# Kernel optimization log

Hardware: AMD Instinct MI355X
Metric: run time of the kernel (lower is better)

## Reference

```python
import jax, jax.numpy as jnp
import numpy as np

N_NODES, N_EDGES, N_GRAPHS = 20000, 320000, 8
NFD, HID, OUT, HEADS = 128, 64, 768, 4


def gat_conv(x, src, dst, ea, W, att_src, att_dst, We, att_edge, bias, heads, concat):
    """PyG GATConv with edge_dim, add_self_loops=True (fill_value='mean'), eval mode."""
    N = x.shape[0]
    H = heads
    C = W.shape[1] // H
    loop = jnp.arange(N, dtype=src.dtype)
    s = jnp.concatenate([src, loop])
    d = jnp.concatenate([dst, loop])
    ea_full = jnp.concatenate([ea, jnp.broadcast_to(ea.mean(axis=0), (N, ea.shape[1]))], axis=0)
    h = (x @ W).reshape(N, H, C)                      # [N,H,C]
    a_s = (h * att_src).sum(-1)                        # [N,H]
    a_d = (h * att_dst).sum(-1)                        # [N,H]
    eh = (ea_full @ We).reshape(-1, H, C)              # [Etot,H,C]
    a_e = (eh * att_edge).sum(-1)                      # [Etot,H]
    logit = jax.nn.leaky_relu(a_s[s] + a_d[d] + a_e, negative_slope=0.2)
    m = jax.ops.segment_max(logit, d, num_segments=N)  # segment softmax over dst
    w = jnp.exp(logit - m[d])
    z = jax.ops.segment_sum(w, d, num_segments=N)
    alpha = w / (z[d] + 1e-16)                         # [Etot,H]
    out = jax.ops.segment_sum(h[s] * alpha[:, :, None], d, num_segments=N)
    out = out.reshape(N, H * C) if concat else out.mean(axis=1)
    return out + bias


def setup_inputs() -> dict:
    key = jax.random.key(0)
    ks = jax.random.split(key, 32)
    p = lambda k, shp: (jax.random.normal(k, shp) * 0.1).astype(jnp.float32)
    inp = {
        'x': jax.random.normal(ks[0], (N_NODES, 5), dtype=jnp.float32),
        'edge_index': jax.random.randint(ks[1], (2, N_EDGES), 0, N_NODES, dtype=jnp.int32),
        'edge_attr': jax.random.uniform(ks[2], (N_EDGES, 4), dtype=jnp.float32),
        'batch': jnp.sort(jax.random.randint(ks[3], (N_NODES,), 0, N_GRAPHS, dtype=jnp.int32)),
        # node_encoder
        'enc_w1': p(ks[4], (5, NFD // 2)), 'enc_b1': jnp.zeros((NFD // 2,), jnp.float32),
        'enc_w2': p(ks[5], (NFD // 2, NFD)), 'enc_b2': jnp.zeros((NFD,), jnp.float32),
        # gat1: in NFD -> HEADS*HID (concat)
        'g1_w': p(ks[6], (NFD, HEADS * HID)), 'g1_asrc': p(ks[7], (HEADS, HID)),
        'g1_adst': p(ks[8], (HEADS, HID)), 'g1_we': p(ks[9], (4, HEADS * HID)),
        'g1_aedge': p(ks[10], (HEADS, HID)), 'g1_b': jnp.zeros((HEADS * HID,), jnp.float32),
        # gat2: in HEADS*HID -> HEADS*HID (concat)
        'g2_w': p(ks[11], (HEADS * HID, HEADS * HID)), 'g2_asrc': p(ks[12], (HEADS, HID)),
        'g2_adst': p(ks[13], (HEADS, HID)), 'g2_we': p(ks[14], (4, HEADS * HID)),
        'g2_aedge': p(ks[15], (HEADS, HID)), 'g2_b': jnp.zeros((HEADS * HID,), jnp.float32),
        # gat3: in HEADS*HID -> HID, heads=1, concat=False
        'g3_w': p(ks[16], (HEADS * HID, HID)), 'g3_asrc': p(ks[17], (1, HID)),
        'g3_adst': p(ks[18], (1, HID)), 'g3_we': p(ks[19], (4, HID)),
        'g3_aedge': p(ks[20], (1, HID)), 'g3_b': jnp.zeros((HID,), jnp.float32),
        # projection HID -> 2*HID -> OUT
        'proj_w1': p(ks[21], (HID, 2 * HID)), 'proj_b1': jnp.zeros((2 * HID,), jnp.float32),
        'proj_w2': p(ks[22], (2 * HID, OUT)), 'proj_b2': jnp.zeros((OUT,), jnp.float32),
        # 5 vulnerability heads stacked: OUT -> 5
        'vuln_w': p(ks[23], (OUT, 5)), 'vuln_b': jnp.zeros((5,), jnp.float32),
    }
    return inp


def reference(x, edge_index, edge_attr, batch,
              enc_w1, enc_b1, enc_w2, enc_b2,
              g1_w, g1_asrc, g1_adst, g1_we, g1_aedge, g1_b,
              g2_w, g2_asrc, g2_adst, g2_we, g2_aedge, g2_b,
              g3_w, g3_asrc, g3_adst, g3_we, g3_aedge, g3_b,
              proj_w1, proj_b1, proj_w2, proj_b2, vuln_w, vuln_b):
    src, dst = edge_index[0], edge_index[1]
    # node_encoder (eval mode, dropout = identity)
    h = jax.nn.relu(x @ enc_w1 + enc_b1)
    h = jax.nn.relu(h @ enc_w2 + enc_b2)                         # [N, NFD]
    # EdgeAwareGAT
    h = jax.nn.elu(gat_conv(h, src, dst, edge_attr, g1_w, g1_asrc, g1_adst, g1_we, g1_aedge, g1_b, HEADS, True))
    h = jax.nn.elu(gat_conv(h, src, dst, edge_attr, g2_w, g2_asrc, g2_adst, g2_we, g2_aedge, g2_b, HEADS, True))
    h = gat_conv(h, src, dst, edge_attr, g3_w, g3_asrc, g3_adst, g3_we, g3_aedge, g3_b, 1, False)  # [N, HID]
    # global_mean_pool
    sums = jax.ops.segment_sum(h, batch, num_segments=N_GRAPHS)
    cnts = jax.ops.segment_sum(jnp.ones((h.shape[0], 1), h.dtype), batch, num_segments=N_GRAPHS)
    g = sums / jnp.maximum(cnts, 1.0)                            # [B, HID]
    # projection
    p1 = jax.nn.relu(g @ proj_w1 + proj_b1)
    static_features = p1 @ proj_w2 + proj_b2                     # [B, OUT]
    scores = jax.nn.sigmoid(static_features @ vuln_w + vuln_b)   # [B, 5]
    return static_features, scores
```

## Files before the change

kernel.cpp:

```cpp
#include <hip/hip_runtime.h>
#include <hip/hip_bf16.h>
#include <hip/hip_fp16.h>
#include <math.h>

#define N_NODES 20000
#define M_PAD 20096
#define N_EDGES 320000
#define N_GRAPHS 8

typedef _Float16 half8 __attribute__((ext_vector_type(8)));
typedef float floatx4 __attribute__((ext_vector_type(4)));

__device__ __forceinline__ float leaky02(float x) { return x > 0.f ? x : 0.2f * x; }
__device__ __forceinline__ float sel4(int hl, float a, float b, float c, float d) {
    return hl < 2 ? (hl == 0 ? a : b) : (hl == 2 ? c : d);
}

__global__ void encoder_kernel(const float* __restrict__ x,
                               const float* __restrict__ w1, const float* __restrict__ b1,
                               const float* __restrict__ w2, const float* __restrict__ b2,
                               __half* __restrict__ out) {
    const int n0 = blockIdx.x * 8;
    const int tid = threadIdx.x;
    __shared__ float s_x[8][5];
    __shared__ float s_h1[8][64];
    if (tid < 40) s_x[tid / 5][tid % 5] = x[(size_t)(n0 + tid / 5) * 5 + (tid % 5)];
    __syncthreads();
    if (tid < 64) {
        #pragma unroll
        for (int n = 0; n < 8; ++n) {
            float a = b1[tid];
            #pragma unroll
            for (int k = 0; k < 5; ++k) a += s_x[n][k] * w1[k * 64 + tid];
            s_h1[n][tid] = fmaxf(a, 0.f);
        }
    }
    __syncthreads();
    float acc[8];
    #pragma unroll
    for (int n = 0; n < 8; ++n) acc[n] = b2[tid];
    for (int k = 0; k < 64; ++k) {
        float wv = w2[k * 128 + tid];
        #pragma unroll
        for (int n = 0; n < 8; ++n) acc[n] += s_h1[n][k] * wv;
    }
    #pragma unroll
    for (int n = 0; n < 8; ++n)
        out[(size_t)(n0 + n) * 128 + tid] = __float2half(fmaxf(acc[n], 0.f));
}

__global__ void ea_sum_kernel(const float* __restrict__ ea, float* __restrict__ ea_sum) {
    const int tid = threadIdx.x;
    float a0 = 0, a1 = 0, a2 = 0, a3 = 0;
    for (int i = blockIdx.x * blockDim.x + tid; i < N_EDGES; i += gridDim.x * blockDim.x) {
        float4 v = ((const float4*)ea)[i];
        a0 += v.x; a1 += v.y; a2 += v.z; a3 += v.w;
    }
    #pragma unroll
    for (int off = 32; off; off >>= 1) {
        a0 += __shfl_down(a0, off, 64);
        a1 += __shfl_down(a1, off, 64);
        a2 += __shfl_down(a2, off, 64);
        a3 += __shfl_down(a3, off, 64);
    }
    __shared__ float s[4][4];
    const int wave = tid >> 6, lane = tid & 63;
    if (lane == 0) { s[wave][0] = a0; s[wave][1] = a1; s[wave][2] = a2; s[wave][3] = a3; }
    __syncthreads();
    if (tid < 4) {
        float t = s[0][tid] + s[1][tid] + s[2][tid] + s[3][tid];
        atomicAdd(&ea_sum[tid], t);
    }
}

__global__ void count_kernel(const int* __restrict__ dst, int* __restrict__ cnt) {
    int i = blockIdx.x * 256 + threadIdx.x;
    if (i < N_EDGES) atomicAdd(&cnt[dst[i]], 1);
}

__global__ void scan_kernel(const int* __restrict__ cnt, int* __restrict__ row_ptr) {
    __shared__ int s_sum[1024];
    const int tid = threadIdx.x;
    int local[20];
    int run = 0;
    const int base = tid * 20;
    #pragma unroll
    for (int i = 0; i < 20; ++i) {
        int idx = base + i;
        int v = (idx < N_NODES) ? cnt[idx] : 0;
        run += v;
        local[i] = run;
    }
    s_sum[tid] = run;
    __syncthreads();
    for (int off = 1; off < 1024; off <<= 1) {
        int v = (tid >= off) ? s_sum[tid - off] : 0;
        __syncthreads();
        s_sum[tid] += v;
        __syncthreads();
    }
    const int prev = (tid > 0) ? s_sum[tid - 1] : 0;
    #pragma unroll
    for (int i = 0; i < 20; ++i) {
        int idx = base + i;
        if (idx < N_NODES) row_ptr[idx + 1] = prev + local[i];
    }
    if (tid == 0) row_ptr[0] = 0;
}

__global__ void scatter_kernel(const int* __restrict__ dst, const int* __restrict__ row_ptr,
                               int* __restrict__ cur, int* __restrict__ eid) {
    int i = blockIdx.x * 256 + threadIdx.x;
    if (i < N_EDGES) {
        int d = dst[i];
        int p = atomicAdd(&cur[d], 1);
        eid[row_ptr[d] + p] = i;
    }
}

__global__ void csr_gather_kernel(const int* __restrict__ srcs, const float* __restrict__ ea,
                                  const int* __restrict__ eids,
                                  int* __restrict__ csr_src, float* __restrict__ csr_ea) {
    int e = blockIdx.x * 256 + threadIdx.x;
    if (e < N_EDGES) {
        int ei = eids[e];
        csr_src[e] = srcs[ei];
        ((float4*)csr_ea)[e] = ((const float4*)ea)[ei];
    }
}

__global__ void wconv_kernel(const float* __restrict__ W, __half* __restrict__ Wt,
                             int K, int N) {
    int i = blockIdx.x * 256 + threadIdx.x;
    if (i < K * N) {
        int k = i / N, n = i % N;
        Wt[(size_t)n * K + k] = __float2half(W[i]);
    }
}

template<int H>
__global__ void vtab_kernel(const float* __restrict__ We, const float* __restrict__ att_edge,
                            const float* __restrict__ ea_sum,
                            float* __restrict__ vtab, float* __restrict__ lpae) {
    const int tid = threadIdx.x;
    __shared__ float s_v[4][4];
    if (tid < 4 * H) {
        const int k = tid / H, h = tid % H;
        float v = 0.f;
        for (int c = 0; c < 64; ++c) v += We[k * (H * 64) + h * 64 + c] * att_edge[h * 64 + c];
        vtab[k * 4 + h] = v;
        s_v[k][h] = v;
    }
    __syncthreads();
    if (tid < H) {
        const float inv = 1.0f / (float)N_EDGES;
        float l = 0.f;
        #pragma unroll
        for (int k = 0; k < 4; ++k) l += ea_sum[k] * inv * s_v[k][tid];
        lpae[tid] = l;
    }
}

template<int N, int H>
__global__ __launch_bounds__(256) void mgemm_kernel(
    const __half* __restrict__ X, const __half* __restrict__ Wt,
    const float* __restrict__ asrc, const float* __restrict__ adst,
    __half* __restrict__ Y, float* __restrict__ a_s, float* __restrict__ a_d, int K) {
    constexpr int STR = 72;
    __shared__ _Float16 sX[64 * STR];
    __shared__ _Float16 sW[64 * STR];
    const int tid = threadIdx.x;
    const int lane = tid & 63, w = tid >> 6;
    const int l16 = lane & 15, kg = lane >> 4;
    const int n0 = blockIdx.x * 64;
    const int c0 = blockIdx.y * 64;
    const int by = blockIdx.y;

    floatx4 acc[4];
    #pragma unroll
    for (int ct = 0; ct < 4; ++ct) acc[ct] = (floatx4){0.f, 0.f, 0.f, 0.f};

    const int srow = tid >> 2, sseg = tid & 3;
    for (int k0 = 0; k0 < K; k0 += 32) {
        float4 xv = *(const float4*)(X + (size_t)(n0 + srow) * K + k0 + sseg * 8);
        float4 wv = *(const float4*)(Wt + (size_t)(c0 + srow) * K + k0 + sseg * 8);
        __syncthreads();
        *(float4*)&sX[srow * STR + sseg * 8] = xv;
        *(float4*)&sW[srow * STR + sseg * 8] = wv;
        __syncthreads();
        half8 a = *(const half8*)&sX[(w * 16 + l16) * STR + kg * 8];
        #pragma unroll
        for (int ct = 0; ct < 4; ++ct) {
            half8 b = *(const half8*)&sW[(ct * 16 + l16) * STR + kg * 8];
            acc[ct] = __builtin_amdgcn_mfma_f32_16x16x32_f16(a, b, acc[ct], 0, 0, 0);
        }
    }

    const int rowb = n0 + w * 16 + kg * 4;
    float ar[4], ad4[4];
    #pragma unroll
    for (int ct = 0; ct < 4; ++ct) {
        ar[ct] = asrc[c0 + ct * 16 + l16];
        ad4[ct] = adst[c0 + ct * 16 + l16];
    }
    #pragma unroll
    for (int ct = 0; ct < 4; ++ct) {
        const int col = c0 + ct * 16 + l16;
        #pragma unroll
        for (int r = 0; r < 4; ++r)
            Y[(size_t)(rowb + r) * N + col] = __float2half(acc[ct][r]);
    }
    #pragma unroll
    for (int r = 0; r < 4; ++r) {
        float p = acc[0][r] * ar[0] + acc[1][r] * ar[1] + acc[2][r] * ar[2] + acc[3][r] * ar[3];
        float q = acc[0][r] * ad4[0] + acc[1][r] * ad4[1] + acc[2][r] * ad4[2] + acc[3][r] * ad4[3];
        #pragma unroll
        for (int off = 1; off < 16; off <<= 1) {
            p += __shfl_xor(p, off, 64);
            q += __shfl_xor(q, off, 64);
        }
        if (l16 == 0) {
            const int node = rowb + r;
            a_s[(size_t)node * H + by] = p;
            a_d[(size_t)node * H + by] = q;
        }
    }
}

template<int H, int HC, bool ELU>
__global__ __launch_bounds__(256) void agg3_kernel(
    const __half* __restrict__ hh,
    const float* __restrict__ a_s, const float* __restrict__ a_d,
    const float* __restrict__ vtab, const float* __restrict__ lpae,
    const int* __restrict__ csr_src, const float* __restrict__ csr_ea,
    const int* __restrict__ row_ptr, const float* __restrict__ bias,
    __half* __restrict__ out) {
    constexpr int CPT = HC / 64;
    const int wave = threadIdx.x >> 6;
    const int lane = threadIdx.x & 63;
    const int d = blockIdx.x * 4 + wave;

    const int base = row_ptr[d], end = row_ptr[d + 1];
    const int colbase = lane * CPT;
    const int hl = (H == 1) ? 0 : (colbase >> 6);

    float vt[4][H];
    #pragma unroll
    for (int k = 0; k < 4; ++k)
        #pragma unroll
        for (int h = 0; h < H; ++h) vt[k][h] = vtab[k * 4 + h];

    float add_[H];
    if (H == 4) {
        float4 t = *(const float4*)&a_d[(size_t)d * 4];
        add_[0] = t.x; add_[1] = t.y; add_[2] = t.z; add_[3] = t.w;
    } else {
        add_[0] = a_d[d];
    }
    float asd_h;
    if (H == 4) asd_h = a_s[(size_t)d * 4 + hl];
    else asd_h = a_s[d];

    float mh = leaky02(asd_h + add_[hl] + lpae[hl]);
    float zacc = 1.f;
    float acc[CPT];
    {
        const __half2* hp = (const __half2*)(hh + (size_t)d * HC + colbase);
        if (CPT == 4) {
            float2 f0 = __half22float2(hp[0]);
            float2 f1 = __half22float2(hp[1]);
            acc[0] = f0.x; acc[1] = f0.y; acc[2] = f1.x; acc[3] = f1.y;
        } else {
            acc[0] = __half2float(hh[(size_t)d * HC + colbase]);
        }
    }

#define EDGE_STEP(tt) { \
        int s_ = __shfl(my_s, (tt), 64); \
        float lt; \
        if (H == 4) { \
            float t0 = __shfl(l0, (tt), 64), t1 = __shfl(l1, (tt), 64); \
            float t2 = __shfl(l2, (tt), 64), t3 = __shfl(l3, (tt), 64); \
            lt = sel4(hl, t0, t1, t2, t3); \
        } else { \
            lt = __shfl(l0, (tt), 64); \
        } \
        float w_ = __expf(lt - mh); \
        const __half2* hp_ = (const __half2*)(hh + (size_t)s_ * HC + colbase); \
        if (CPT == 4) { \
            float2 f0_ = __half22float2(hp_[0]); \
            float2 f1_ = __half22float2(hp_[1]); \
            acc[0] += w_ * f0_.x; acc[1] += w_ * f0_.y; \
            acc[2] += w_ * f1_.x; acc[3] += w_ * f1_.y; \
        } else { \
            acc[0] += w_ * __half2float(hh[(size_t)s_ * HC + colbase]); \
        } \
        zacc += w_; }

    for (int c0 = base; c0 < end; c0 += 64) {
        const int nc = min(64, end - c0);
        int my_s = 0;
        float l0 = -1e30f, l1 = -1e30f, l2 = -1e30f, l3 = -1e30f;
        if (lane < nc) {
            my_s = csr_src[c0 + lane];
            float4 eav = ((const float4*)csr_ea)[c0 + lane];
            if (H == 4) {
                float4 as4 = *(const float4*)&a_s[(size_t)my_s * 4];
                l0 = leaky02(as4.x + add_[0] + eav.x * vt[0][0] + eav.y * vt[1][0] + eav.z * vt[2][0] + eav.w * vt[3][0]);
                l1 = leaky02(as4.y + add_[1] + eav.x * vt[0][1] + eav.y * vt[1][1] + eav.z * vt[2][1] + eav.w * vt[3][1]);
                l2 = leaky02(as4.z + add_[2] + eav.x * vt[0][2] + eav.y * vt[1][2] + eav.z * vt[2][2] + eav.w * vt[3][2]);
                l3 = leaky02(as4.w + add_[3] + eav.x * vt[0][3] + eav.y * vt[1][3] + eav.z * vt[2][3] + eav.w * vt[3][3]);
            } else {
                l0 = leaky02(a_s[my_s] + add_[0] + eav.x * vt[0][0] + eav.y * vt[1][0] + eav.z * vt[2][0] + eav.w * vt[3][0]);
            }
        }
        float cm0 = l0, cm1 = l1, cm2 = l2, cm3 = l3;
        #pragma unroll
        for (int off = 1; off < 64; off <<= 1) {
            cm0 = fmaxf(cm0, __shfl_xor(cm0, off, 64));
            if (H == 4) {
                cm1 = fmaxf(cm1, __shfl_xor(cm1, off, 64));
                cm2 = fmaxf(cm2, __shfl_xor(cm2, off, 64));
                cm3 = fmaxf(cm3, __shfl_xor(cm3, off, 64));
            }
        }
        float cmh = (H == 4) ? sel4(hl, cm0, cm1, cm2, cm3) : cm0;
        float newm = fmaxf(mh, cmh);
        float sc = __expf(mh - newm);
        zacc *= sc;
        #pragma unroll
        for (int c = 0; c < CPT; ++c) acc[c] *= sc;
        mh = newm;

        int t = 0;
        for (; t + 4 <= nc; t += 4) {
            EDGE_STEP(t)
            EDGE_STEP(t + 1)
            EDGE_STEP(t + 2)
            EDGE_STEP(t + 3)
        }
        for (; t < nc; ++t) {
            EDGE_STEP(t)
        }
    }
#undef EDGE_STEP

    const float invz = 1.f / (zacc + 1e-16f);
    #pragma unroll
    for (int c = 0; c < CPT; ++c) {
        float v = acc[c] * invz + bias[colbase + c];
        if (ELU) v = (v > 0.f) ? v : (__expf(v) - 1.f);
        acc[c] = v;
    }
    if (CPT == 4) {
        __half2* op = (__half2*)(out + (size_t)d * HC + colbase);
        op[0] = __floats2half2_rn(acc[0], acc[1]);
        op[1] = __floats2half2_rn(acc[2], acc[3]);
    } else {
        out[(size_t)d * HC + colbase] = __float2half(acc[0]);
    }
}

__global__ void pool_kernel(const __half* __restrict__ h3, const int* __restrict__ batch,
                            float* __restrict__ psum, float* __restrict__ pcnt) {
    __shared__ float s_acc[8][64];
    __shared__ float s_cnt[8];
    const int tid = threadIdx.x;
    for (int i = tid; i < 512; i += 256) s_acc[i >> 6][i & 63] = 0.f;
    if (tid < 8) s_cnt[tid] = 0.f;
    __syncthreads();
    const int col = tid & 63, nl = tid >> 6;
    const int n0 = blockIdx.x * 64;
    for (int nn = nl; nn < 64; nn += 4) {
        int n = n0 + nn;
        if (n < N_NODES) {
            int b = batch[n];
            atomicAdd(&s_acc[b][col], __half2float(h3[(size_t)n * 64 + col]));
            if (col == 0) atomicAdd(&s_cnt[b], 1.0f);
        }
    }
    __syncthreads();
    for (int i = tid; i < 512; i += 256) {
        float v = s_acc[i >> 6][i & 63];
        if (v != 0.f) atomicAdd(&psum[i], v);
    }
    if (tid < 8 && s_cnt[tid] > 0.f) atomicAdd(&pcnt[tid], s_cnt[tid]);
}

__global__ void head_sf_kernel(const float* __restrict__ psum, const float* __restrict__ pcnt,
                               const float* __restrict__ w1, const float* __restrict__ b1,
                               const float* __restrict__ w2, const float* __restrict__ b2,
                               float* __restrict__ out) {
    const int b = blockIdx.y;
    const int c0 = blockIdx.x * 128;
    const int tid = threadIdx.x;
    __shared__ float s_g[64];
    __shared__ float s_p1[128];
    if (tid < 64) {
        float c = pcnt[b];
        c = (c < 1.f) ? 1.f : c;
        s_g[tid] = psum[b * 64 + tid] / c;
    }
    __syncthreads();
    {
        float a = b1[tid];
        #pragma unroll 8
        for (int k = 0; k < 64; ++k) a += s_g[k] * w1[k * 128 + tid];
        s_p1[tid] = fmaxf(a, 0.f);
    }
    __syncthreads();
    const int col = c0 + tid;
    float a = b2[col];
    #pragma unroll 8
    for (int k = 0; k < 128; ++k) a += s_p1[k] * w2[k * 768 + col];
    out[b * 768 + col] = a;
}

__global__ void scores_kernel(const float* __restrict__ sf,
                              const float* __restrict__ vw, const float* __restrict__ vb,
                              float* __restrict__ out) {
    const int b = blockIdx.x;
    const int tid = threadIdx.x;
    const int wave = tid >> 6, lane = tid & 63;
    float part[5] = {0.f, 0.f, 0.f, 0.f, 0.f};
    for (int k = tid; k < 768; k += 256) {
        float s = sf[b * 768 + k];
        #pragma unroll
        for (int v = 0; v < 5; ++v) part[v] += s * vw[k * 5 + v];
    }
    #pragma unroll
    for (int v = 0; v < 5; ++v)
        #pragma unroll
        for (int off = 32; off; off >>= 1) part[v] += __shfl_down(part[v], off, 64);
    __shared__ float sred[4][5];
    if (lane == 0) {
        #pragma unroll
        for (int v = 0; v < 5; ++v) sred[wave][v] = part[v];
    }
    __syncthreads();
    if (tid < 5) {
        float a = vb[tid] + sred[0][tid] + sred[1][tid] + sred[2][tid] + sred[3][tid];
        out[6144 + b * 5 + tid] = 1.f / (1.f + __expf(-a));
    }
}

extern "C" void kernel_launch(void* const* d_in, const int* in_sizes, int n_in,
                              void* d_out, int out_size, void* d_ws, size_t ws_size,
                              hipStream_t stream) {
    const float* x       = (const float*)d_in[0];
    const int*   eidx    = (const int*)d_in[1];
    const float* ea      = (const float*)d_in[2];
    const int*   batch   = (const int*)d_in[3];
    const float* enc_w1  = (const float*)d_in[4];
    const float* enc_b1  = (const float*)d_in[5];
    const float* enc_w2  = (const float*)d_in[6];
    const float* enc_b2  = (const float*)d_in[7];
    const float* g1_w    = (const float*)d_in[8];
    const float* g1_asrc = (const float*)d_in[9];
    const float* g1_adst = (const float*)d_in[10];
    const float* g1_we   = (const float*)d_in[11];
    const float* g1_ae   = (const float*)d_in[12];
    const float* g1_b    = (const float*)d_in[13];
    const float* g2_w    = (const float*)d_in[14];
    const float* g2_asrc = (const float*)d_in[15];
    const float* g2_adst = (const float*)d_in[16];
    const float* g2_we   = (const float*)d_in[17];
    const float* g2_ae   = (const float*)d_in[18];
    const float* g2_b    = (const float*)d_in[19];
    const float* g3_w    = (const float*)d_in[20];
    const float* g3_asrc = (const float*)d_in[21];
    const float* g3_adst = (const float*)d_in[22];
    const float* g3_we   = (const float*)d_in[23];
    const float* g3_ae   = (const float*)d_in[24];
    const float* g3_b    = (const float*)d_in[25];
    const float* pw1     = (const float*)d_in[26];
    const float* pb1     = (const float*)d_in[27];
    const float* pw2     = (const float*)d_in[28];
    const float* pb2     = (const float*)d_in[29];
    const float* vw      = (const float*)d_in[30];
    const float* vb      = (const float*)d_in[31];

    const int* src = eidx;
    const int* dst = eidx + N_EDGES;

    __half* h16a = (__half*)d_ws;
    __half* h16b = h16a + (size_t)M_PAD * 256;
    __half* hh16 = h16b + (size_t)M_PAD * 256;
    __half* wt16 = hh16 + (size_t)M_PAD * 256;
    float* asb   = (float*)(wt16 + 256 * 256);
    float* adb   = asb + (size_t)M_PAD * 4;
    float* zreg  = adb + (size_t)M_PAD * 4;
    float* ea_sum = zreg;
    float* psum   = zreg + 4;
    float* pcnt   = zreg + 516;
    float* vtab  = zreg + 524;
    float* lpae  = vtab + 16;
    int* icnt    = (int*)(lpae + 4);
    int* icur    = icnt + N_NODES;
    int* irow    = icur + N_NODES;
    int* ieid    = irow + N_NODES + 4;
    int* csr_src = ieid + N_EDGES;
    float* csr_ea = (float*)(csr_src + N_EDGES);

    hipMemsetAsync(zreg, 0, 544 * sizeof(float), stream);
    hipMemsetAsync(icnt, 0, 2 * N_NODES * sizeof(int), stream);

    ea_sum_kernel<<<256, 256, 0, stream>>>(ea, ea_sum);
    encoder_kernel<<<N_NODES / 8, 128, 0, stream>>>(x, enc_w1, enc_b1, enc_w2, enc_b2, h16a);
    count_kernel<<<(N_EDGES + 255) / 256, 256, 0, stream>>>(dst, icnt);
    scan_kernel<<<1, 1024, 0, stream>>>(icnt, irow);
    scatter_kernel<<<(N_EDGES + 255) / 256, 256, 0, stream>>>(dst, irow, icur, ieid);
    csr_gather_kernel<<<(N_EDGES + 255) / 256, 256, 0, stream>>>(src, ea, ieid, csr_src, csr_ea);

    wconv_kernel<<<(128 * 256 + 255) / 256, 256, 0, stream>>>(g1_w, wt16, 128, 256);
    vtab_kernel<4><<<1, 64, 0, stream>>>(g1_we, g1_ae, ea_sum, vtab, lpae);
    mgemm_kernel<256, 4><<<dim3(M_PAD / 64, 4), 256, 0, stream>>>(h16a, wt16, g1_asrc, g1_adst, hh16, asb, adb, 128);
    agg3_kernel<4, 256, true><<<N_NODES / 4, 256, 0, stream>>>(hh16, asb, adb, vtab, lpae, csr_src, csr_ea, irow, g1_b, h16b);

    wconv_kernel<<<(256 * 256 + 255) / 256, 256, 0, stream>>>(g2_w, wt16, 256, 256);
    vtab_kernel<4><<<1, 64, 0, stream>>>(g2_we, g2_ae, ea_sum, vtab, lpae);
    mgemm_kernel<256, 4><<<dim3(M_PAD / 64, 4), 256, 0, stream>>>(h16b, wt16, g2_asrc, g2_adst, hh16, asb, adb, 256);
    agg3_kernel<4, 256, true><<<N_NODES / 4, 256, 0, stream>>>(hh16, asb, adb, vtab, lpae, csr_src, csr_ea, irow, g2_b, h16a);

    wconv_kernel<<<(256 * 64 + 255) / 256, 256, 0, stream>>>(g3_w, wt16, 256, 64);
    vtab_kernel<1><<<1, 64, 0, stream>>>(g3_we, g3_ae, ea_sum, vtab, lpae);
    mgemm_kernel<64, 1><<<dim3(M_PAD / 64, 1), 256, 0, stream>>>(h16a, wt16, g3_asrc, g3_adst, hh16, asb, adb, 256);
    agg3_kernel<1, 64, false><<<N_NODES / 4, 256, 0, stream>>>(hh16, asb, adb, vtab, lpae, csr_src, csr_ea, irow, g3_b, h16b);

    pool_kernel<<<(N_NODES + 63) / 64, 256, 0, stream>>>(h16b, batch, psum, pcnt);
    head_sf_kernel<<<dim3(6, 8), 128, 0, stream>>>(psum, pcnt, pw1, pb1, pw2, pb2, (float*)d_out);
    scores_kernel<<<8, 256, 0, stream>>>((float*)d_out, vw, vb, (float*)d_out);
}
```

Before: 337.3 us.

## Fuse preprocessing kernels, drop online softmax max, widen GEMM K step

Edge counting moves into the edge-attribute sum kernel, and the CSR scatter now writes source ids and edge attributes directly, so the separate eid gather pass goes away. The three weight conversions and the three vtab computations become one launch each. The GEMM loads 64 K-elements per shared-memory stage instead of 32, and the aggregation kernel unrolls by 8. The aggregation softmax now uses each node's self-loop logit as a fixed shift instead of a running max, which removes the per-chunk wave max reductions and rescaling. Without the max shift, exp can overflow if an edge logit is much larger than the self-loop logit.

```diff
diff --git a/kernel.cpp b/kernel.cpp
--- a/kernel.cpp
+++ b/kernel.cpp
@@ -10,6 +10,8 @@
 
 typedef _Float16 half8 __attribute__((ext_vector_type(8)));
 typedef float floatx4 __attribute__((ext_vector_type(4)));
+
+struct h4pack { __half2 a, b; };
 
 __device__ __forceinline__ float leaky02(float x) { return x > 0.f ? x : 0.2f * x; }
 __device__ __forceinline__ float sel4(int hl, float a, float b, float c, float d) {
@@ -49,12 +51,14 @@
         out[(size_t)(n0 + n) * 128 + tid] = __float2half(fmaxf(acc[n], 0.f));
 }
 
-__global__ void ea_sum_kernel(const float* __restrict__ ea, float* __restrict__ ea_sum) {
+__global__ void prep_kernel(const float* __restrict__ ea, const int* __restrict__ dst,
+                            float* __restrict__ ea_sum, int* __restrict__ cnt) {
     const int tid = threadIdx.x;
     float a0 = 0, a1 = 0, a2 = 0, a3 = 0;
     for (int i = blockIdx.x * blockDim.x + tid; i < N_EDGES; i += gridDim.x * blockDim.x) {
         float4 v = ((const float4*)ea)[i];
         a0 += v.x; a1 += v.y; a2 += v.z; a3 += v.w;
+        atomicAdd(&cnt[dst[i]], 1);
     }
     #pragma unroll
     for (int off = 32; off; off >>= 1) {
@@ -73,11 +77,6 @@
     }
 }
 
-__global__ void count_kernel(const int* __restrict__ dst, int* __restrict__ cnt) {
-    int i = blockIdx.x * 256 + threadIdx.x;
-    if (i < N_EDGES) atomicAdd(&cnt[dst[i]], 1);
-}
-
 __global__ void scan_kernel(const int* __restrict__ cnt, int* __restrict__ row_ptr) {
     __shared__ int s_sum[1024];
     const int tid = threadIdx.x;
@@ -108,56 +107,64 @@
     if (tid == 0) row_ptr[0] = 0;
 }
 
-__global__ void scatter_kernel(const int* __restrict__ dst, const int* __restrict__ row_ptr,
-                               int* __restrict__ cur, int* __restrict__ eid) {
+__global__ void scatter_kernel(const int* __restrict__ src, const int* __restrict__ dst,
+                               const float* __restrict__ ea,
+                               const int* __restrict__ row_ptr, int* __restrict__ cur,
+                               int* __restrict__ csr_src, float* __restrict__ csr_ea) {
     int i = blockIdx.x * 256 + threadIdx.x;
     if (i < N_EDGES) {
         int d = dst[i];
         int p = atomicAdd(&cur[d], 1);
-        eid[row_ptr[d] + p] = i;
-    }
-}
-
-__global__ void csr_gather_kernel(const int* __restrict__ srcs, const float* __restrict__ ea,
-                                  const int* __restrict__ eids,
-                                  int* __restrict__ csr_src, float* __restrict__ csr_ea) {
-    int e = blockIdx.x * 256 + threadIdx.x;
-    if (e < N_EDGES) {
-        int ei = eids[e];
-        csr_src[e] = srcs[ei];
-        ((float4*)csr_ea)[e] = ((const float4*)ea)[ei];
-    }
-}
-
-__global__ void wconv_kernel(const float* __restrict__ W, __half* __restrict__ Wt,
-                             int K, int N) {
+        int idx = row_ptr[d] + p;
+        csr_src[idx] = src[i];
+        ((float4*)csr_ea)[idx] = ((const float4*)ea)[i];
+    }
+}
+
+__global__ void wconv_all_kernel(const float* __restrict__ w1, const float* __restrict__ w2,
+                                 const float* __restrict__ w3,
+                                 __half* __restrict__ wt1, __half* __restrict__ wt2,
+                                 __half* __restrict__ wt3) {
     int i = blockIdx.x * 256 + threadIdx.x;
-    if (i < K * N) {
-        int k = i / N, n = i % N;
-        Wt[(size_t)n * K + k] = __float2half(W[i]);
-    }
-}
-
-template<int H>
-__global__ void vtab_kernel(const float* __restrict__ We, const float* __restrict__ att_edge,
-                            const float* __restrict__ ea_sum,
-                            float* __restrict__ vtab, float* __restrict__ lpae) {
-    const int tid = threadIdx.x;
-    __shared__ float s_v[4][4];
+    if (i < 32768) {
+        int k = i >> 8, n = i & 255;
+        wt1[(size_t)n * 128 + k] = __float2half(w1[i]);
+    } else if (i < 98304) {
+        int j = i - 32768;
+        int k = j >> 8, n = j & 255;
+        wt2[(size_t)n * 256 + k] = __float2half(w2[j]);
+    } else if (i < 114688) {
+        int j = i - 98304;
+        int k = j >> 6, n = j & 63;
+        wt3[(size_t)n * 256 + k] = __float2half(w3[j]);
+    }
+}
+
+__global__ void vtab_all_kernel(const float* __restrict__ we1, const float* __restrict__ ae1,
+                                const float* __restrict__ we2, const float* __restrict__ ae2,
+                                const float* __restrict__ we3, const float* __restrict__ ae3,
+                                const float* __restrict__ ea_sum,
+                                float* __restrict__ vtab, float* __restrict__ lpae) {
+    const int L = blockIdx.x;
+    const float* We = (L == 0) ? we1 : ((L == 1) ? we2 : we3);
+    const float* Ae = (L == 0) ? ae1 : ((L == 1) ? ae2 : ae3);
+    const int H = (L < 2) ? 4 : 1;
+    const int tid = threadIdx.x;
+    __shared__ float s_v[16];
     if (tid < 4 * H) {
         const int k = tid / H, h = tid % H;
         float v = 0.f;
-        for (int c = 0; c < 64; ++c) v += We[k * (H * 64) + h * 64 + c] * att_edge[h * 64 + c];
-        vtab[k * 4 + h] = v;
-        s_v[k][h] = v;
+        for (int c = 0; c < 64; ++c) v += We[k * (H * 64) + h * 64 + c] * Ae[h * 64 + c];
+        vtab[L * 16 + k * 4 + h] = v;
+        s_v[k * 4 + h] = v;
     }
     __syncthreads();
     if (tid < H) {
         const float inv = 1.0f / (float)N_EDGES;
         float l = 0.f;
         #pragma unroll
-        for (int k = 0; k < 4; ++k) l += ea_sum[k] * inv * s_v[k][tid];
-        lpae[tid] = l;
+        for (int k = 0; k < 4; ++k) l += ea_sum[k] * inv * s_v[k * 4 + tid];
+        lpae[L * 4 + tid] = l;
     }
 }
 
@@ -181,18 +188,25 @@
     for (int ct = 0; ct < 4; ++ct) acc[ct] = (floatx4){0.f, 0.f, 0.f, 0.f};
 
     const int srow = tid >> 2, sseg = tid & 3;
-    for (int k0 = 0; k0 < K; k0 += 32) {
-        float4 xv = *(const float4*)(X + (size_t)(n0 + srow) * K + k0 + sseg * 8);
-        float4 wv = *(const float4*)(Wt + (size_t)(c0 + srow) * K + k0 + sseg * 8);
+    for (int k0 = 0; k0 < K; k0 += 64) {
+        float4 xv0 = *(const float4*)(X + (size_t)(n0 + srow) * K + k0 + sseg * 8);
+        float4 xv1 = *(const float4*)(X + (size_t)(n0 + srow) * K + k0 + 32 + sseg * 8);
+        float4 wv0 = *(const float4*)(Wt + (size_t)(c0 + srow) * K + k0 + sseg * 8);
+        float4 wv1 = *(const float4*)(Wt + (size_t)(c0 + srow) * K + k0 + 32 + sseg * 8);
         __syncthreads();
-        *(float4*)&sX[srow * STR + sseg * 8] = xv;
-        *(float4*)&sW[srow * STR + sseg * 8] = wv;
+        *(float4*)&sX[srow * STR + sseg * 8] = xv0;
+        *(float4*)&sX[srow * STR + 32 + sseg * 8] = xv1;
+        *(float4*)&sW[srow * STR + sseg * 8] = wv0;
+        *(float4*)&sW[srow * STR + 32 + sseg * 8] = wv1;
         __syncthreads();
-        half8 a = *(const half8*)&sX[(w * 16 + l16) * STR + kg * 8];
-        #pragma unroll
-        for (int ct = 0; ct < 4; ++ct) {
-            half8 b = *(const half8*)&sW[(ct * 16 + l16) * STR + kg * 8];
-            acc[ct] = __builtin_amdgcn_mfma_f32_16x16x32_f16(a, b, acc[ct], 0, 0, 0);
+        #pragma unroll
+        for (int ks = 0; ks < 2; ++ks) {
+            half8 a = *(const half8*)&sX[(w * 16 + l16) * STR + ks * 32 + kg * 8];
+            #pragma unroll
+            for (int ct = 0; ct < 4; ++ct) {
+                half8 b = *(const half8*)&sW[(ct * 16 + l16) * STR + ks * 32 + kg * 8];
+                acc[ct] = __builtin_amdgcn_mfma_f32_16x16x32_f16(a, b, acc[ct], 0, 0, 0);
+            }
         }
     }
 
@@ -228,7 +242,7 @@
 }
 
 template<int H, int HC, bool ELU>
-__global__ __launch_bounds__(256) void agg3_kernel(
+__global__ __launch_bounds__(256) void agg4_kernel(
     const __half* __restrict__ hh,
     const float* __restrict__ a_s, const float* __restrict__ a_d,
     const float* __restrict__ vtab, const float* __restrict__ lpae,
@@ -250,46 +264,45 @@
         #pragma unroll
         for (int h = 0; h < H; ++h) vt[k][h] = vtab[k * 4 + h];
 
-    float add_[H];
+    float add_[H], lself[H];
     if (H == 4) {
         float4 t = *(const float4*)&a_d[(size_t)d * 4];
         add_[0] = t.x; add_[1] = t.y; add_[2] = t.z; add_[3] = t.w;
+        float4 s4 = *(const float4*)&a_s[(size_t)d * 4];
+        lself[0] = leaky02(s4.x + add_[0] + lpae[0]);
+        lself[1] = leaky02(s4.y + add_[1] + lpae[1]);
+        lself[2] = leaky02(s4.z + add_[2] + lpae[2]);
+        lself[3] = leaky02(s4.w + add_[3] + lpae[3]);
     } else {
         add_[0] = a_d[d];
-    }
-    float asd_h;
-    if (H == 4) asd_h = a_s[(size_t)d * 4 + hl];
-    else asd_h = a_s[d];
-
-    float mh = leaky02(asd_h + add_[hl] + lpae[hl]);
+        lself[0] = leaky02(a_s[d] + add_[0] + lpae[0]);
+    }
+
     float zacc = 1.f;
     float acc[CPT];
-    {
-        const __half2* hp = (const __half2*)(hh + (size_t)d * HC + colbase);
-        if (CPT == 4) {
-            float2 f0 = __half22float2(hp[0]);
-            float2 f1 = __half22float2(hp[1]);
-            acc[0] = f0.x; acc[1] = f0.y; acc[2] = f1.x; acc[3] = f1.y;
-        } else {
-            acc[0] = __half2float(hh[(size_t)d * HC + colbase]);
-        }
+    if (CPT == 4) {
+        h4pack hv = *(const h4pack*)(hh + (size_t)d * HC + colbase);
+        float2 f0 = __half22float2(hv.a);
+        float2 f1 = __half22float2(hv.b);
+        acc[0] = f0.x; acc[1] = f0.y; acc[2] = f1.x; acc[3] = f1.y;
+    } else {
+        acc[0] = __half2float(hh[(size_t)d * HC + colbase]);
     }
 
 #define EDGE_STEP(tt) { \
         int s_ = __shfl(my_s, (tt), 64); \
-        float lt; \
+        float w_; \
         if (H == 4) { \
-            float t0 = __shfl(l0, (tt), 64), t1 = __shfl(l1, (tt), 64); \
-            float t2 = __shfl(l2, (tt), 64), t3 = __shfl(l3, (tt), 64); \
-            lt = sel4(hl, t0, t1, t2, t3); \
+            float t0 = __shfl(w0, (tt), 64), t1 = __shfl(w1, (tt), 64); \
+            float t2 = __shfl(w2, (tt), 64), t3 = __shfl(w3, (tt), 64); \
+            w_ = sel4(hl, t0, t1, t2, t3); \
         } else { \
-            lt = __shfl(l0, (tt), 64); \
+            w_ = __shfl(w0, (tt), 64); \
         } \
-        float w_ = __expf(lt - mh); \
-        const __half2* hp_ = (const __half2*)(hh + (size_t)s_ * HC + colbase); \
         if (CPT == 4) { \
-            float2 f0_ = __half22float2(hp_[0]); \
-            float2 f1_ = __half22float2(hp_[1]); \
+            h4pack hv_ = *(const h4pack*)(hh + (size_t)s_ * HC + colbase); \
+            float2 f0_ = __half22float2(hv_.a); \
+            float2 f1_ = __half22float2(hv_.b); \
             acc[0] += w_ * f0_.x; acc[1] += w_ * f0_.y; \
             acc[2] += w_ * f1_.x; acc[3] += w_ * f1_.y; \
         } else { \
@@ -300,44 +313,35 @@
     for (int c0 = base; c0 < end; c0 += 64) {
         const int nc = min(64, end - c0);
         int my_s = 0;
-        float l0 = -1e30f, l1 = -1e30f, l2 = -1e30f, l3 = -1e30f;
+        float w0 = 0.f, w1 = 0.f, w2 = 0.f, w3 = 0.f;
         if (lane < nc) {
             my_s = csr_src[c0 + lane];
             float4 eav = ((const float4*)csr_ea)[c0 + lane];
             if (H == 4) {
                 float4 as4 = *(const float4*)&a_s[(size_t)my_s * 4];
-                l0 = leaky02(as4.x + add_[0] + eav.x * vt[0][0] + eav.y * vt[1][0] + eav.z * vt[2][0] + eav.w * vt[3][0]);
-                l1 = leaky02(as4.y + add_[1] + eav.x * vt[0][1] + eav.y * vt[1][1] + eav.z * vt[2][1] + eav.w * vt[3][1]);
-                l2 = leaky02(as4.z + add_[2] + eav.x * vt[0][2] + eav.y * vt[1][2] + eav.z * vt[2][2] + eav.w * vt[3][2]);
-                l3 = leaky02(as4.w + add_[3] + eav.x * vt[0][3] + eav.y * vt[1][3] + eav.z * vt[2][3] + eav.w * vt[3][3]);
+                float l0 = leaky02(as4.x + add_[0] + eav.x * vt[0][0] + eav.y * vt[1][0] + eav.z * vt[2][0] + eav.w * vt[3][0]);
+                float l1 = leaky02(as4.y + add_[1] + eav.x * vt[0][1] + eav.y * vt[1][1] + eav.z * vt[2][1] + eav.w * vt[3][1]);
+                float l2 = leaky02(as4.z + add_[2] + eav.x * vt[0][2] + eav.y * vt[1][2] + eav.z * vt[2][2] + eav.w * vt[3][2]);
+                float l3 = leaky02(as4.w + add_[3] + eav.x * vt[0][3] + eav.y * vt[1][3] + eav.z * vt[2][3] + eav.w * vt[3][3]);
+                w0 = __expf(l0 - lself[0]);
+                w1 = __expf(l1 - lself[1]);
+                w2 = __expf(l2 - lself[2]);
+                w3 = __expf(l3 - lself[3]);
             } else {
-                l0 = leaky02(a_s[my_s] + add_[0] + eav.x * vt[0][0] + eav.y * vt[1][0] + eav.z * vt[2][0] + eav.w * vt[3][0]);
+                float l0 = leaky02(a_s[my_s] + add_[0] + eav.x * vt[0][0] + eav.y * vt[1][0] + eav.z * vt[2][0] + eav.w * vt[3][0]);
+                w0 = __expf(l0 - lself[0]);
             }
         }
-        float cm0 = l0, cm1 = l1, cm2 = l2, cm3 = l3;
-        #pragma unroll
-        for (int off = 1; off < 64; off <<= 1) {
-            cm0 = fmaxf(cm0, __shfl_xor(cm0, off, 64));
-            if (H == 4) {
-                cm1 = fmaxf(cm1, __shfl_xor(cm1, off, 64));
-                cm2 = fmaxf(cm2, __shfl_xor(cm2, off, 64));
-                cm3 = fmaxf(cm3, __shfl_xor(cm3, off, 64));
-            }
-        }
-        float cmh = (H == 4) ? sel4(hl, cm0, cm1, cm2, cm3) : cm0;
-        float newm = fmaxf(mh, cmh);
-        float sc = __expf(mh - newm);
-        zacc *= sc;
-        #pragma unroll
-        for (int c = 0; c < CPT; ++c) acc[c] *= sc;
-        mh = newm;
-
         int t = 0;
-        for (; t + 4 <= nc; t += 4) {
+        for (; t + 8 <= nc; t += 8) {
             EDGE_STEP(t)
             EDGE_STEP(t + 1)
             EDGE_STEP(t + 2)
             EDGE_STEP(t + 3)
+            EDGE_STEP(t + 4)
+            EDGE_STEP(t + 5)
+            EDGE_STEP(t + 6)
+            EDGE_STEP(t + 7)
         }
         for (; t < nc; ++t) {
             EDGE_STEP(t)
@@ -486,46 +490,41 @@
     __half* h16a = (__half*)d_ws;
     __half* h16b = h16a + (size_t)M_PAD * 256;
     __half* hh16 = h16b + (size_t)M_PAD * 256;
-    __half* wt16 = hh16 + (size_t)M_PAD * 256;
-    float* asb   = (float*)(wt16 + 256 * 256);
+    __half* wt1  = hh16 + (size_t)M_PAD * 256;
+    __half* wt2  = wt1 + 32768;
+    __half* wt3  = wt2 + 65536;
+    float* asb   = (float*)(wt3 + 16384);
     float* adb   = asb + (size_t)M_PAD * 4;
     float* zreg  = adb + (size_t)M_PAD * 4;
     float* ea_sum = zreg;
     float* psum   = zreg + 4;
     float* pcnt   = zreg + 516;
-    float* vtab  = zreg + 524;
-    float* lpae  = vtab + 16;
-    int* icnt    = (int*)(lpae + 4);
+    float* vtab   = zreg + 524;
+    float* lpae   = zreg + 572;
+    int* icnt    = (int*)(zreg + 584);
     int* icur    = icnt + N_NODES;
     int* irow    = icur + N_NODES;
-    int* ieid    = irow + N_NODES + 4;
-    int* csr_src = ieid + N_EDGES;
+    int* csr_src = irow + N_NODES + 16;
     float* csr_ea = (float*)(csr_src + N_EDGES);
 
-    hipMemsetAsync(zreg, 0, 544 * sizeof(float), stream);
+    hipMemsetAsync(zreg, 0, 584 * sizeof(float), stream);
     hipMemsetAsync(icnt, 0, 2 * N_NODES * sizeof(int), stream);
 
-    ea_sum_kernel<<<256, 256, 0, stream>>>(ea, ea_sum);
+    prep_kernel<<<256, 256, 0, stream>>>(ea, dst, ea_sum, icnt);
     encoder_kernel<<<N_NODES / 8, 128, 0, stream>>>(x, enc_w1, enc_b1, enc_w2, enc_b2, h16a);
-    count_kernel<<<(N_EDGES + 255) / 256, 256, 0, stream>>>(dst, icnt);
     scan_kernel<<<1, 1024, 0, stream>>>(icnt, irow);
-    scatter_kernel<<<(N_EDGES + 255) / 256, 256, 0, stream>>>(dst, irow, icur, ieid);
-    csr_gather_kernel<<<(N_EDGES + 255) / 256, 256, 0, stream>>>(src, ea, ieid, csr_src, csr_ea);
-
-    wconv_kernel<<<(128 * 256 + 255) / 256, 256, 0, stream>>>(g1_w, wt16, 128, 256);
-    vtab_kernel<4><<<1, 64, 0, stream>>>(g1_we, g1_ae, ea_sum, vtab, lpae);
-    mgemm_kernel<256, 4><<<dim3(M_PAD / 64, 4), 256, 0, stream>>>(h16a, wt16, g1_asrc, g1_adst, hh16, asb, adb, 128);
-    agg3_kernel<4, 256, true><<<N_NODES / 4, 256, 0, stream>>>(hh16, asb, adb, vtab, lpae, csr_src, csr_ea, irow, g1_b, h16b);
-
-    wconv_kernel<<<(256 * 256 + 255) / 256, 256, 0, stream>>>(g2_w, wt16, 256, 256);
-    vtab_kernel<4><<<1, 64, 0, stream>>>(g2_we, g2_ae, ea_sum, vtab, lpae);
-    mgemm_kernel<256, 4><<<dim3(M_PAD / 64, 4), 256, 0, stream>>>(h16b, wt16, g2_asrc, g2_adst, hh16, asb, adb, 256);
-    agg3_kernel<4, 256, true><<<N_NODES / 4, 256, 0, stream>>>(hh16, asb, adb, vtab, lpae, csr_src, csr_ea, irow, g2_b, h16a);
-
-    wconv_kernel<<<(256 * 64 + 255) / 256, 256, 0, stream>>>(g3_w, wt16, 256, 64);
-    vtab_kernel<1><<<1, 64, 0, stream>>>(g3_we, g3_ae, ea_sum, vtab, lpae);
-    mgemm_kernel<64, 1><<<dim3(M_PAD / 64, 1), 256, 0, stream>>>(h16a, wt16, g3_asrc, g3_adst, hh16, asb, adb, 256);
-    agg3_kernel<1, 64, false><<<N_NODES / 4, 256, 0, stream>>>(hh16, asb, adb, vtab, lpae, csr_src, csr_ea, irow, g3_b, h16b);
+    scatter_kernel<<<(N_EDGES + 255) / 256, 256, 0, stream>>>(src, dst, ea, irow, icur, csr_src, csr_ea);
+    wconv_all_kernel<<<448, 256, 0, stream>>>(g1_w, g2_w, g3_w, wt1, wt2, wt3);
+    vtab_all_kernel<<<3, 64, 0, stream>>>(g1_we, g1_ae, g2_we, g2_ae, g3_we, g3_ae, ea_sum, vtab, lpae);
+
+    mgemm_kernel<256, 4><<<dim3(M_PAD / 64, 4), 256, 0, stream>>>(h16a, wt1, g1_asrc, g1_adst, hh16, asb, adb, 128);
+    agg4_kernel<4, 256, true><<<N_NODES / 4, 256, 0, stream>>>(hh16, asb, adb, vtab, lpae, csr_src, csr_ea, irow, g1_b, h16b);
+
+    mgemm_kernel<256, 4><<<dim3(M_PAD / 64, 4), 256, 0, stream>>>(h16b, wt2, g2_asrc, g2_adst, hh16, asb, adb, 256);
+    agg4_kernel<4, 256, true><<<N_NODES / 4, 256, 0, stream>>>(hh16, asb, adb, vtab + 16, lpae + 4, csr_src, csr_ea, irow, g2_b, h16a);
+
+    mgemm_kernel<64, 1><<<dim3(M_PAD / 64, 1), 256, 0, stream>>>(h16a, wt3, g3_asrc, g3_adst, hh16, asb, adb, 256);
+    agg4_kernel<1, 64, false><<<N_NODES / 4, 256, 0, stream>>>(hh16, asb, adb, vtab + 32, lpae + 8, csr_src, csr_ea, irow, g3_b, h16b);
 
     pool_kernel<<<(N_NODES + 63) / 64, 256, 0, stream>>>(h16b, batch, psum, pcnt);
     head_sf_kernel<<<dim3(6, 8), 128, 0, stream>>>(psum, pcnt, pw1, pb1, pw2, pb2, (float*)d_out);
```

Result: slower. 1.019 ms (+202.1%).
